# Performance work log

Measured on AMD Instinct MI355X. Metric: run time of the kernel, lower is better.

## Reference

```python
import jax, jax.numpy as jnp
import numpy as np

ALPHA = 0.1   # synaptic current decay
BETA = 0.96   # membrane decay
V_THR = 2.0   # firing threshold


def setup_inputs() -> dict:
    key = jax.random.key(0)
    T, B, N = 512, 32, 4096
    x = jax.random.normal(key, (T, B, N), dtype=jnp.float32)
    return {"x": x}


def reference(x):
    """snntorch Synaptic neuron scan, reset_mechanism='zero'.

    Per step (snntorch semantics):
      reset   = heaviside(mem_prev - thr)           (spike from previous mem)
      syn'    = alpha*syn + x_t
      mem'    = beta*mem + syn'
      zero reset: syn' -= reset*syn'; mem' -= reset*mem'
      spk     = heaviside(mem' - thr)
    """
    dt = x.dtype

    def step(carry, xt):
        syn, mem = carry
        reset = (mem > V_THR).astype(dt)
        syn_n = ALPHA * syn + xt
        mem_n = BETA * mem + syn_n
        syn_n = syn_n * (1.0 - reset)
        mem_n = mem_n * (1.0 - reset)
        spk = (mem_n > V_THR).astype(dt)
        return (syn_n, mem_n), (spk, syn_n, mem_n)

    init = (jnp.zeros_like(x[0]), jnp.zeros_like(x[0]))
    _, (spk, syn, mem) = jax.lax.scan(step, init, x)
    return spk, syn, mem
```

## Files before the change

kernel.cpp:

```cpp
#include <hip/hip_runtime.h>


#define T_STEPS 512
#define BN      131072

__global__ __launch_bounds__(256) void snn_synaptic_kernel(
    const float* __restrict__ x, float* __restrict__ out) {
  const int i = blockIdx.x * 256 + threadIdx.x;

  float* __restrict__ spk_o = out;
  float* __restrict__ syn_o = out + (long long)T_STEPS * BN;
  float* __restrict__ mem_o = out + 2LL * T_STEPS * BN;

  float syn = 0.f, mem = 0.f;

  float x0 = x[i];
  float x1 = x[1 * BN + i];
  float x2 = x[2 * BN + i];
  float x3 = x[3 * BN + i];

  for (int t = 0; t < T_STEPS; t += 4) {
    const int pb = ((t + 4 < T_STEPS) ? (t + 4) : t) * BN + i;
    const float n0 = x[pb];
    const float n1 = x[pb + BN];
    const float n2 = x[pb + 2 * BN];
    const float n3 = x[pb + 3 * BN];

    #define STEP(tt, XV)                                           \
      {                                                            \
        const float keep = (mem > 2.0f) ? 0.0f : 1.0f;             \
        syn = __fadd_rn(__fmul_rn(0.1f, syn), XV);                 \
        mem = __fadd_rn(__fmul_rn(0.96f, mem), syn);               \
        syn *= keep;                                               \
        mem *= keep;                                               \
        const float spk = (mem > 2.0f) ? 1.0f : 0.0f;              \
        const int o = (tt) * BN + i;                               \
        __builtin_nontemporal_store(spk, spk_o + o);               \
        __builtin_nontemporal_store(syn, syn_o + o);               \
        __builtin_nontemporal_store(mem, mem_o + o);               \
      }
    STEP(t + 0, x0) STEP(t + 1, x1) STEP(t + 2, x2) STEP(t + 3, x3)
    #undef STEP

    x0 = n0; x1 = n1; x2 = n2; x3 = n3;
  }
}

extern "C" void kernel_launch(void* const* d_in, const int* in_sizes, int n_in,
                              void* d_out, int out_size, void* d_ws, size_t ws_size,
                              hipStream_t stream) {
  const float* x = (const float*)d_in[0];
  float* out = (float*)d_out;
  snn_synaptic_kernel<<<dim3(BN / 256), dim3(256), 0, stream>>>(x, out);
}
```

Baseline: 954.9 us.

## Deepen prefetch to 16 timesteps and switch to regular cached stores

Raises the software-pipelined prefetch depth from 4 to 16 timesteps of x per thread, so more loads are in flight to hide memory latency in the serial scan. Replaces the nontemporal stores with plain stores. Empty asm barriers keep all 48 per-block output values live in registers, which likely pushes the stores to the end of each block and batches them. This raises register pressure and may reduce occupancy; dropping the nontemporal hint may change cache behaviour for the large write stream.

```diff
diff --git a/kernel.cpp b/kernel.cpp
--- a/kernel.cpp
+++ b/kernel.cpp
@@ -3,6 +3,9 @@
 
 #define T_STEPS 512
 #define BN      131072
+
+#define REPEAT16(M) M(0) M(1) M(2) M(3) M(4) M(5) M(6) M(7) \
+                    M(8) M(9) M(10) M(11) M(12) M(13) M(14) M(15)
 
 __global__ __launch_bounds__(256) void snn_synaptic_kernel(
     const float* __restrict__ x, float* __restrict__ out) {
@@ -14,35 +17,53 @@
 
   float syn = 0.f, mem = 0.f;
 
-  float x0 = x[i];
-  float x1 = x[1 * BN + i];
-  float x2 = x[2 * BN + i];
-  float x3 = x[3 * BN + i];
+  #define DECLXP(s) float xp##s = x[(s) * BN + i];
+  REPEAT16(DECLXP)
+  #undef DECLXP
 
-  for (int t = 0; t < T_STEPS; t += 4) {
-    const int pb = ((t + 4 < T_STEPS) ? (t + 4) : t) * BN + i;
-    const float n0 = x[pb];
-    const float n1 = x[pb + BN];
-    const float n2 = x[pb + 2 * BN];
-    const float n3 = x[pb + 3 * BN];
+  for (int tb = 0; tb < T_STEPS; tb += 16) {
+    const int nb = ((tb + 16) & (T_STEPS - 1)) * BN + i;
 
-    #define STEP(tt, XV)                                           \
-      {                                                            \
-        const float keep = (mem > 2.0f) ? 0.0f : 1.0f;             \
-        syn = __fadd_rn(__fmul_rn(0.1f, syn), XV);                 \
-        mem = __fadd_rn(__fmul_rn(0.96f, mem), syn);               \
-        syn *= keep;                                               \
-        mem *= keep;                                               \
-        const float spk = (mem > 2.0f) ? 1.0f : 0.0f;              \
-        const int o = (tt) * BN + i;                               \
-        __builtin_nontemporal_store(spk, spk_o + o);               \
-        __builtin_nontemporal_store(syn, syn_o + o);               \
-        __builtin_nontemporal_store(mem, mem_o + o);               \
+    #define LOADN(s) const float xn##s = x[nb + (s) * BN];
+    REPEAT16(LOADN)
+    #undef LOADN
+
+    const int ob = tb * BN + i;
+
+    #define STEP(s)                                                  \
+      const float keep##s = (mem > 2.0f) ? 0.0f : 1.0f;              \
+      syn = __fadd_rn(__fmul_rn(0.1f, syn), xp##s);                  \
+      mem = __fadd_rn(__fmul_rn(0.96f, mem), syn);                   \
+      syn *= keep##s;                                                \
+      mem *= keep##s;                                                \
+      const float q_spk##s = (mem > 2.0f) ? 1.0f : 0.0f;             \
+      const float q_syn##s = syn;                                    \
+      const float q_mem##s = mem;                                    \
+      {                                                              \
+        const int o = ob + (s) * BN;                                 \
+        spk_o[o] = q_spk##s;                                         \
+        syn_o[o] = q_syn##s;                                         \
+        mem_o[o] = q_mem##s;                                         \
       }
-    STEP(t + 0, x0) STEP(t + 1, x1) STEP(t + 2, x2) STEP(t + 3, x3)
+    REPEAT16(STEP)
     #undef STEP
 
-    x0 = n0; x1 = n1; x2 = n2; x3 = n3;
+    asm volatile("" :: "v"(q_spk0),  "v"(q_spk1),  "v"(q_spk2),  "v"(q_spk3),
+                       "v"(q_spk4),  "v"(q_spk5),  "v"(q_spk6),  "v"(q_spk7),
+                       "v"(q_spk8),  "v"(q_spk9),  "v"(q_spk10), "v"(q_spk11),
+                       "v"(q_spk12), "v"(q_spk13), "v"(q_spk14), "v"(q_spk15));
+    asm volatile("" :: "v"(q_syn0),  "v"(q_syn1),  "v"(q_syn2),  "v"(q_syn3),
+                       "v"(q_syn4),  "v"(q_syn5),  "v"(q_syn6),  "v"(q_syn7),
+                       "v"(q_syn8),  "v"(q_syn9),  "v"(q_syn10), "v"(q_syn11),
+                       "v"(q_syn12), "v"(q_syn13), "v"(q_syn14), "v"(q_syn15));
+    asm volatile("" :: "v"(q_mem0),  "v"(q_mem1),  "v"(q_mem2),  "v"(q_mem3),
+                       "v"(q_mem4),  "v"(q_mem5),  "v"(q_mem6),  "v"(q_mem7),
+                       "v"(q_mem8),  "v"(q_mem9),  "v"(q_mem10), "v"(q_mem11),
+                       "v"(q_mem12), "v"(q_mem13), "v"(q_mem14), "v"(q_mem15));
+
+    #define ROT(s) xp##s = xn##s;
+    REPEAT16(ROT)
+    #undef ROT
   }
 }
 
```

New measurement: 966.4 us. Within noise of the previous version (+1.2%).
